# Kernel tuning notes

Hardware: AMD Instinct MI355X
Metric: run time of the kernel (lower is better)

Reference implementation:

```python
import jax, jax.numpy as jnp
import numpy as np

EPS = 1e-8  # torch nn.CosineSimilarity default eps


def setup_inputs() -> dict:
    key = jax.random.key(0)
    k1, k2 = jax.random.split(key)
    support_set = jax.random.normal(k1, (50000, 512), dtype=jnp.float32)
    query_set = jax.random.normal(k2, (2048, 512), dtype=jnp.float32)
    return {"support_set": support_set, "query_set": query_set}


def reference(support_set, query_set):
    # torch: cos(x1, x2) = x1.x2 / max(||x1|| * ||x2||, eps), per row.
    # Loop over queries fused into one matmul: out[q, n] = cos(support[n], query[q]).
    dots = jnp.einsum("qd,nd->qn", query_set, support_set)        # [Q, N]
    s_norm = jnp.linalg.norm(support_set, axis=1)                  # [N]
    q_norm = jnp.linalg.norm(query_set, axis=1)                    # [Q]
    denom = jnp.maximum(q_norm[:, None] * s_norm[None, :], EPS)    # [Q, N]
    return dots / denom
```

## Files before the change

kernel.cpp:

```cpp
#include <hip/hip_runtime.h>
#include <stdint.h>

#define NSUP   50000
#define NSUPP  50176
#define NQRY   2048
#define KD     512
#define BK     32
#define NKT    16

typedef __attribute__((ext_vector_type(8))) short bf16x8;
typedef __attribute__((ext_vector_type(4))) float f32x4;

__device__ __forceinline__ unsigned short f2bf(float f) {
  unsigned int u = __float_as_uint(f);
  u += 0x7FFFu + ((u >> 16) & 1u);
  return (unsigned short)(u >> 16);
}

__global__ __launch_bounds__(256) void prep_kernel(
    const float* __restrict__ sup, const float* __restrict__ qry,
    unsigned short* __restrict__ s_bf, unsigned short* __restrict__ q_bf) {
  const int row  = blockIdx.x * 4 + (threadIdx.x >> 6);
  const int lane = threadIdx.x & 63;

  const float* src = nullptr;
  unsigned short* dst;
  if (row < NSUPP) {
    dst = s_bf + (size_t)row * KD;
    if (row < NSUP) src = sup + (size_t)row * KD;
  } else {
    const int r = row - NSUPP;
    dst = q_bf + (size_t)r * KD;
    src = qry + (size_t)r * KD;
  }

  if (src == nullptr) {
    bf16x8 z = {};
    *(bf16x8*)(dst + lane * 8) = z;
    return;
  }

  const float4 v0 = ((const float4*)src)[lane * 2 + 0];
  const float4 v1 = ((const float4*)src)[lane * 2 + 1];
  float ss = v0.x*v0.x + v0.y*v0.y + v0.z*v0.z + v0.w*v0.w
           + v1.x*v1.x + v1.y*v1.y + v1.z*v1.z + v1.w*v1.w;
  #pragma unroll
  for (int off = 32; off > 0; off >>= 1) ss += __shfl_xor(ss, off);
  const float inv = rsqrtf(fmaxf(ss, 1e-30f));

  bf16x8 o;
  o[0]=(short)f2bf(v0.x*inv); o[1]=(short)f2bf(v0.y*inv);
  o[2]=(short)f2bf(v0.z*inv); o[3]=(short)f2bf(v0.w*inv);
  o[4]=(short)f2bf(v1.x*inv); o[5]=(short)f2bf(v1.y*inv);
  o[6]=(short)f2bf(v1.z*inv); o[7]=(short)f2bf(v1.w*inv);
  *(bf16x8*)(dst + lane * 8) = o;
}

__device__ __forceinline__ void stage_tile(const unsigned short* __restrict__ g,
                                           unsigned short* lds, int grow_base,
                                           int kt, int w, int l) {
  const int chunk = (l & 3) ^ ((l >> 3) & 3);
  #pragma unroll
  for (int i = 0; i < 2; ++i) {
    const unsigned short* src = g + (size_t)(grow_base + i*128 + w*16 + (l>>2)) * KD
                                  + kt*BK + chunk*8;
    unsigned short* dst = lds + i*4096 + w*512;
    __builtin_amdgcn_global_load_lds(
        (const __attribute__((address_space(1))) void*)src,
        (__attribute__((address_space(3))) void*)dst, 16, 0, 0);
  }
}

#define SWZ_OFF(R, hi) (((hi) ^ (((R) >> 1) & 3)) * 8)

__global__ __launch_bounds__(512, 1) void gemm_kernel(
    const unsigned short* __restrict__ S,
    const unsigned short* __restrict__ Q,
    float* __restrict__ out) {
  __shared__ __attribute__((aligned(16))) unsigned short As[3][256][BK];
  __shared__ __attribute__((aligned(16))) unsigned short Bs[3][256][BK];

  const int tid = threadIdx.x;
  const int w = tid >> 6, l = tid & 63;
  const int wm = w >> 2, wn = w & 3;
  const int rof = l & 15, hi = l >> 4;

  int bid = blockIdx.y * 196 + blockIdx.x;
  bid = (bid & 7) * 196 + (bid >> 3);
  const int ts = (bid % 196) * 256;
  const int tq = (bid / 196) * 256;

  f32x4 acc[8][4] = {};

  stage_tile(S, &As[0][0][0], ts, 0, w, l);
  stage_tile(Q, &Bs[0][0][0], tq, 0, w, l);
  stage_tile(S, &As[1][0][0], ts, 1, w, l);
  stage_tile(Q, &Bs[1][0][0], tq, 1, w, l);
  asm volatile("s_waitcnt vmcnt(4)" ::: "memory");
  __builtin_amdgcn_s_barrier();
  asm volatile("" ::: "memory");

  #pragma unroll
  for (int t = 0; t < NKT; ++t) {
    const int slot  = t % 3;
    const int nslot = (t + 2) % 3;
    const int nkt   = (t + 2) & 15;

    stage_tile(S, &As[nslot][0][0], ts, nkt, w, l);
    stage_tile(Q, &Bs[nslot][0][0], tq, nkt, w, l);

    bf16x8 a[8], b[4];
    #pragma unroll
    for (int i = 0; i < 8; ++i) {
      const int R = wm*128 + i*16 + rof;
      a[i] = *(const bf16x8*)&As[slot][R][SWZ_OFF(R, hi)];
    }
    #pragma unroll
    for (int i = 0; i < 4; ++i) {
      const int R = wn*64 + i*16 + rof;
      b[i] = *(const bf16x8*)&Bs[slot][R][SWZ_OFF(R, hi)];
    }

    __builtin_amdgcn_s_setprio(1);
    #pragma unroll
    for (int mi = 0; mi < 8; ++mi)
      #pragma unroll
      for (int ni = 0; ni < 4; ++ni)
        acc[mi][ni] = __builtin_amdgcn_mfma_f32_16x16x32_bf16(a[mi], b[ni], acc[mi][ni], 0, 0, 0);
    __builtin_amdgcn_s_setprio(0);

    asm volatile("s_waitcnt vmcnt(4)" ::: "memory");
    __builtin_amdgcn_s_barrier();
    asm volatile("" ::: "memory");
  }

  #pragma unroll
  for (int mi = 0; mi < 8; ++mi) {
    const int s = ts + wm*128 + mi*16 + hi*4;
    if (s < NSUP) {
      #pragma unroll
      for (int ni = 0; ni < 4; ++ni) {
        const int q = tq + wn*64 + ni*16 + rof;
        *(f32x4*)(out + (size_t)q * NSUP + s) = acc[mi][ni];
      }
    }
  }
}

extern "C" void kernel_launch(void* const* d_in, const int* in_sizes, int n_in,
                              void* d_out, int out_size, void* d_ws, size_t ws_size,
                              hipStream_t stream) {
  const float* sup = (const float*)d_in[0];
  const float* qry = (const float*)d_in[1];
  float* out = (float*)d_out;

  char* ws = (char*)d_ws;
  unsigned short* s_bf = (unsigned short*)(ws);
  unsigned short* q_bf = (unsigned short*)(ws + (size_t)NSUPP * KD * 2);

  prep_kernel<<<(NSUPP + NQRY) / 4, 256, 0, stream>>>(sup, qry, s_bf, q_bf);

  dim3 grid(196, 8);
  gemm_kernel<<<grid, 512, 0, stream>>>(s_bf, q_bf, out);
}
```

Measured before the change: 242.0 us.

## Shrink GEMM tile to 128x128 with 4 waves and double buffering

Replaces the 256x256 block tile (8 waves, triple-buffered LDS, explicit vmcnt waits, setprio) with a 128x128 tile run by 4 waves, a double buffer and plain __syncthreads. Launch bounds let 3 blocks share a CU and the grid grows to 392x16, aiming for more occupancy and better load balance across CUs. In exchange each loaded element is reused less, so global and LDS traffic per FLOP goes up, and the full-barrier sync with no prefetch depth may stall on memory latency.

Measured after the change: 246.5 us. About the same (+1.8%).

```diff
diff --git a/kernel.cpp b/kernel.cpp
--- a/kernel.cpp
+++ b/kernel.cpp
@@ -56,15 +56,15 @@
   *(bf16x8*)(dst + lane * 8) = o;
 }
 
-__device__ __forceinline__ void stage_tile(const unsigned short* __restrict__ g,
+__device__ __forceinline__ void stage_unit(const unsigned short* __restrict__ g,
                                            unsigned short* lds, int grow_base,
                                            int kt, int w, int l) {
   const int chunk = (l & 3) ^ ((l >> 3) & 3);
   #pragma unroll
   for (int i = 0; i < 2; ++i) {
-    const unsigned short* src = g + (size_t)(grow_base + i*128 + w*16 + (l>>2)) * KD
+    const unsigned short* src = g + (size_t)(grow_base + i*64 + w*16 + (l>>2)) * KD
                                   + kt*BK + chunk*8;
-    unsigned short* dst = lds + i*4096 + w*512;
+    unsigned short* dst = lds + i*2048 + w*512;
     __builtin_amdgcn_global_load_lds(
         (const __attribute__((address_space(1))) void*)src,
         (__attribute__((address_space(3))) void*)dst, 16, 0, 0);
@@ -73,74 +73,65 @@
 
 #define SWZ_OFF(R, hi) (((hi) ^ (((R) >> 1) & 3)) * 8)
 
-__global__ __launch_bounds__(512, 1) void gemm_kernel(
+__global__ __launch_bounds__(256, 3) void gemm_kernel(
     const unsigned short* __restrict__ S,
     const unsigned short* __restrict__ Q,
     float* __restrict__ out) {
-  __shared__ __attribute__((aligned(16))) unsigned short As[3][256][BK];
-  __shared__ __attribute__((aligned(16))) unsigned short Bs[3][256][BK];
+  __shared__ __attribute__((aligned(16))) unsigned short As[2][128][BK];
+  __shared__ __attribute__((aligned(16))) unsigned short Bs[2][128][BK];
 
   const int tid = threadIdx.x;
   const int w = tid >> 6, l = tid & 63;
-  const int wm = w >> 2, wn = w & 3;
+  const int wr = w >> 1, wc = w & 1;
   const int rof = l & 15, hi = l >> 4;
 
-  int bid = blockIdx.y * 196 + blockIdx.x;
-  bid = (bid & 7) * 196 + (bid >> 3);
-  const int ts = (bid % 196) * 256;
-  const int tq = (bid / 196) * 256;
+  int bid = blockIdx.y * 392 + blockIdx.x;
+  bid = (bid & 7) * 784 + (bid >> 3);
+  const int ts = (bid % 392) * 128;
+  const int tq = (bid / 392) * 128;
 
-  f32x4 acc[8][4] = {};
+  f32x4 acc[4][4] = {};
 
-  stage_tile(S, &As[0][0][0], ts, 0, w, l);
-  stage_tile(Q, &Bs[0][0][0], tq, 0, w, l);
-  stage_tile(S, &As[1][0][0], ts, 1, w, l);
-  stage_tile(Q, &Bs[1][0][0], tq, 1, w, l);
-  asm volatile("s_waitcnt vmcnt(4)" ::: "memory");
-  __builtin_amdgcn_s_barrier();
-  asm volatile("" ::: "memory");
+  stage_unit(S, &As[0][0][0], ts, 0, w, l);
+  stage_unit(Q, &Bs[0][0][0], tq, 0, w, l);
+  __syncthreads();
 
   #pragma unroll
   for (int t = 0; t < NKT; ++t) {
-    const int slot  = t % 3;
-    const int nslot = (t + 2) % 3;
-    const int nkt   = (t + 2) & 15;
+    const int slot = t & 1;
+    if (t + 1 < NKT) {
+      stage_unit(S, &As[slot ^ 1][0][0], ts, t + 1, w, l);
+      stage_unit(Q, &Bs[slot ^ 1][0][0], tq, t + 1, w, l);
+    }
 
-    stage_tile(S, &As[nslot][0][0], ts, nkt, w, l);
-    stage_tile(Q, &Bs[nslot][0][0], tq, nkt, w, l);
-
-    bf16x8 a[8], b[4];
+    bf16x8 a[4], b[4];
     #pragma unroll
-    for (int i = 0; i < 8; ++i) {
-      const int R = wm*128 + i*16 + rof;
+    for (int i = 0; i < 4; ++i) {
+      const int R = wr*64 + i*16 + rof;
       a[i] = *(const bf16x8*)&As[slot][R][SWZ_OFF(R, hi)];
     }
     #pragma unroll
     for (int i = 0; i < 4; ++i) {
-      const int R = wn*64 + i*16 + rof;
+      const int R = wc*64 + i*16 + rof;
       b[i] = *(const bf16x8*)&Bs[slot][R][SWZ_OFF(R, hi)];
     }
 
-    __builtin_amdgcn_s_setprio(1);
     #pragma unroll
-    for (int mi = 0; mi < 8; ++mi)
+    for (int mi = 0; mi < 4; ++mi)
       #pragma unroll
       for (int ni = 0; ni < 4; ++ni)
         acc[mi][ni] = __builtin_amdgcn_mfma_f32_16x16x32_bf16(a[mi], b[ni], acc[mi][ni], 0, 0, 0);
-    __builtin_amdgcn_s_setprio(0);
 
-    asm volatile("s_waitcnt vmcnt(4)" ::: "memory");
-    __builtin_amdgcn_s_barrier();
-    asm volatile("" ::: "memory");
+    __syncthreads();
   }
 
   #pragma unroll
-  for (int mi = 0; mi < 8; ++mi) {
-    const int s = ts + wm*128 + mi*16 + hi*4;
+  for (int mi = 0; mi < 4; ++mi) {
+    const int s = ts + wr*64 + mi*16 + hi*4;
     if (s < NSUP) {
       #pragma unroll
       for (int ni = 0; ni < 4; ++ni) {
-        const int q = tq + wn*64 + ni*16 + rof;
+        const int q = tq + wc*64 + ni*16 + rof;
         *(f32x4*)(out + (size_t)q * NSUP + s) = acc[mi][ni];
       }
     }
@@ -160,6 +151,6 @@
 
   prep_kernel<<<(NSUPP + NQRY) / 4, 256, 0, stream>>>(sup, qry, s_bf, q_bf);
 
-  dim3 grid(196, 8);
-  gemm_kernel<<<grid, 512, 0, stream>>>(s_bf, q_bf, out);
+  dim3 grid(392, 16);
+  gemm_kernel<<<grid, 256, 0, stream>>>(s_bf, q_bf, out);
 }
```
